# Performance work log

Measured on AMD Instinct MI355X. Metric: run time of the kernel, lower is better.

The kernel has to match this reference:

```python
import jax, jax.numpy as jnp
import numpy as np

B, S, E, H = 4, 2048, 2048, 16
D = E // H  # head_dim = 128
ROPE_BASE = 10000.0


def rope(x, base=ROPE_BASE, offset=0):
    # x: (..., seq, d) with interleaved even/odd rotation
    d = x.shape[-1]
    s = x.shape[-2]
    inv_freq = base ** (-jnp.arange(0, d, 2, dtype=jnp.float32) / d)  # (d/2,)
    pos = jnp.arange(offset, s + offset, dtype=jnp.float32)  # (s,)
    ang = pos[:, None] * inv_freq  # (s, d/2)
    sin, cos = jnp.sin(ang), jnp.cos(ang)
    xe, xo = x[..., 0::2], x[..., 1::2]
    re = xe * cos - xo * sin
    ro = xe * sin + xo * cos
    return jnp.stack([re, ro], axis=-1).reshape(x.shape)


def setup_inputs() -> dict:
    key = jax.random.key(0)
    ks = jax.random.split(key, 9)
    w = lambda k, shp: jax.random.normal(k, shp, dtype=jnp.float32) * 0.02
    return {
        "x": jax.random.normal(ks[0], (B, S, E), dtype=jnp.float32),
        "Wq": w(ks[1], (E, E)), "bq": w(ks[2], (E,)),
        "Wk": w(ks[3], (E, E)), "bk": w(ks[4], (E,)),
        "Wv": w(ks[5], (E, E)), "bv": w(ks[6], (E,)),
        "Wo": w(ks[7], (E, E)), "bo": w(ks[8], (E,)),
    }


def reference(x, Wq, bq, Wk, bk, Wv, bv, Wo, bo):
    b, s, _ = x.shape
    scale = D ** -0.5
    # torch Linear: y = x @ W.T + b
    def proj(W, bias):
        y = jnp.einsum('bse,fe->bsf', x, W) + bias
        return y.reshape(b, s, H, D).transpose(0, 2, 1, 3)  # (b, h, s, d)
    q = rope(proj(Wq, bq))
    k = rope(proj(Wk, bk))
    v = proj(Wv, bv)
    attn = jnp.einsum('bhqd,bhkd->bhqk', q, k) * scale  # (b, h, s, s)
    causal = jnp.triu(jnp.ones((s, s), dtype=bool), k=1)
    attn = jnp.where(causal, -jnp.inf, attn)
    attn_weights = jax.nn.softmax(attn, axis=-1)
    out = jnp.einsum('bhqk,bhkd->bhqd', attn_weights, v)
    out = out.transpose(0, 2, 1, 3).reshape(b, s, E)
    return jnp.einsum('bse,fe->bsf', out, Wo) + bo
```

## Files before the change

kernel.cpp:

```cpp
#include <hip/hip_runtime.h>
#include <hip/hip_bf16.h>
#include <stdint.h>

#define B_ 4
#define S_ 2048
#define E_ 2048
#define H_ 16
#define D_ 128
#define M_ (B_ * S_)

typedef unsigned short ushort_t;
typedef unsigned int uint_t;
typedef __attribute__((ext_vector_type(4))) float f32x4;
typedef __attribute__((ext_vector_type(8))) short bf16x8;

__device__ __forceinline__ ushort_t f2bf(float f) {
  uint_t u = __float_as_uint(f);
  u += 0x7FFFu + ((u >> 16) & 1u);
  return (ushort_t)(u >> 16);
}
__device__ __forceinline__ float bf2f(ushort_t h) {
  return __uint_as_float(((uint_t)h) << 16);
}
__device__ __forceinline__ uint_t cvt_pk_bf16(float lo, float hi) {
  uint_t r;
  asm("v_cvt_pk_bf16_f32 %0, %1, %2" : "=v"(r) : "v"(lo), "v"(hi));
  return r;
}

#define GLOAD_LDS16(gp, lp)                                   \
  __builtin_amdgcn_global_load_lds(                           \
      (__attribute__((address_space(1))) void*)(gp),          \
      (__attribute__((address_space(3))) void*)(lp), 16, 0, 0)

__global__ void f32_to_bf16(const float* __restrict__ in, ushort_t* __restrict__ out,
                            size_t n4) {
  const size_t stride = (size_t)gridDim.x * blockDim.x;
  for (size_t i = (size_t)blockIdx.x * blockDim.x + threadIdx.x; i < n4; i += stride) {
    float4 f = ((const float4*)in)[i];
    uint_t lo = (uint_t)f2bf(f.x) | ((uint_t)f2bf(f.y) << 16);
    uint_t hi = (uint_t)f2bf(f.z) | ((uint_t)f2bf(f.w) << 16);
    ((uint2*)out)[i] = make_uint2(lo, hi);
  }
}

__global__ void rope_k(ushort_t* __restrict__ T) {
  const size_t total = (size_t)M_ * (E_ / 8);
  const size_t stride = (size_t)gridDim.x * blockDim.x;
  for (size_t c = (size_t)blockIdx.x * blockDim.x + threadIdx.x; c < total; c += stride) {
    const int row = (int)(c >> 8);
    const int ch = (int)(c & 255);
    const int s = row & (S_ - 1);
    const int p0 = ((ch * 8) & (D_ - 1)) >> 1;
    ushort_t* p = T + ((size_t)row << 11) + ch * 8;
    bf16x8 v = *(bf16x8*)p;
#pragma unroll
    for (int j = 0; j < 4; j++) {
      const int ip = p0 + j;
      const float inv = __expf(-0.14391156963595867f * (float)ip);
      const float ang = (float)s * inv;
      float sn, cs;
      sincosf(ang, &sn, &cs);
      const float xe = bf2f((ushort_t)v[2 * j]);
      const float xo = bf2f((ushort_t)v[2 * j + 1]);
      v[2 * j] = (short)f2bf(xe * cs - xo * sn);
      v[2 * j + 1] = (short)f2bf(xe * sn + xo * cs);
    }
    *(bf16x8*)p = v;
  }
}

__global__ __launch_bounds__(256) void transpose_v(const ushort_t* __restrict__ Vp,
                                                   ushort_t* __restrict__ Vt) {
  const int b = blockIdx.z, h = blockIdx.y;
  const int s0 = blockIdx.x * 64;
  const int tid = threadIdx.x;
  __shared__ ushort_t T[64][136];
#pragma unroll
  for (int i = 0; i < 4; i++) {
    const int c = i * 256 + tid;
    const int s = c >> 4, d8 = c & 15;
    *(bf16x8*)(&T[s][d8 * 8]) =
        *(const bf16x8*)(Vp + (size_t)(b * S_ + s0 + s) * E_ + h * D_ + d8 * 8);
  }
  __syncthreads();
#pragma unroll
  for (int i = 0; i < 4; i++) {
    const int c = i * 256 + tid;
    const int d = c >> 3, s8 = c & 7;
    bf16x8 v;
#pragma unroll
    for (int j = 0; j < 8; j++) v[j] = (short)T[s8 * 8 + j][d];
    *(bf16x8*)(Vt + ((size_t)(b * H_ + h) * D_ + d) * S_ + s0 + s8 * 8) = v;
  }
}

template <int OUTF32>
__global__ __launch_bounds__(256, 2) void gemm_bt(const ushort_t* __restrict__ A,
                                                  const ushort_t* __restrict__ Bw,
                                                  const float* __restrict__ bias,
                                                  void* __restrict__ Cv) {
  __shared__ ushort_t As[128 * 64];
  __shared__ ushort_t Bs[128 * 64];
  const int tid = threadIdx.x;
  const int w = tid >> 6, l = tid & 63, g = l >> 4, ln = l & 15;
  const int wm = w >> 1, wn = w & 1;
  const int flat = blockIdx.y * 16 + blockIdx.x;
  const int swz = (flat & 7) * 128 + (flat >> 3);
  const int m0 = (swz >> 4) * 128, n0 = (swz & 15) * 128;

  f32x4 acc[4][4];
#pragma unroll
  for (int i = 0; i < 4; i++)
#pragma unroll
    for (int j = 0; j < 4; j++)
#pragma unroll
      for (int r = 0; r < 4; r++) acc[i][j][r] = 0.f;

  const ushort_t* Ab = A + (size_t)m0 * E_;
  const ushort_t* Bb = Bw + (size_t)n0 * E_;

  for (int k0 = 0; k0 < E_; k0 += 64) {
    __syncthreads();
#pragma unroll
    for (int i = 0; i < 4; i++) {
      const int c = i * 256 + tid;
      const int row = c >> 3;
      const int gs = (c & 7) ^ (row & 7);
      GLOAD_LDS16(Ab + (size_t)row * E_ + k0 + gs * 8, (char*)As + (i * 256 + w * 64) * 16);
      GLOAD_LDS16(Bb + (size_t)row * E_ + k0 + gs * 8, (char*)Bs + (i * 256 + w * 64) * 16);
    }
    __syncthreads();
#pragma unroll
    for (int kk = 0; kk < 2; kk++) {
      bf16x8 af[4], bfr[4];
#pragma unroll
      for (int mi = 0; mi < 4; mi++) {
        const int row = wm * 64 + mi * 16 + ln;
        const int sl = (kk * 4 + g) ^ (row & 7);
        af[mi] = *(const bf16x8*)(As + row * 64 + sl * 8);
      }
#pragma unroll
      for (int ni = 0; ni < 4; ni++) {
        const int row = wn * 64 + ni * 16 + ln;
        const int sl = (kk * 4 + g) ^ (row & 7);
        bfr[ni] = *(const bf16x8*)(Bs + row * 64 + sl * 8);
      }
#pragma unroll
      for (int mi = 0; mi < 4; mi++)
#pragma unroll
        for (int ni = 0; ni < 4; ni++)
          acc[mi][ni] =
              __builtin_amdgcn_mfma_f32_16x16x32_bf16(af[mi], bfr[ni], acc[mi][ni], 0, 0, 0);
    }
  }

  float bv[4];
#pragma unroll
  for (int ni = 0; ni < 4; ni++) bv[ni] = bias[n0 + wn * 64 + ni * 16 + ln];
#pragma unroll
  for (int mi = 0; mi < 4; mi++)
#pragma unroll
    for (int ni = 0; ni < 4; ni++)
#pragma unroll
      for (int r = 0; r < 4; r++) {
        const float v = acc[mi][ni][r] + bv[ni];
        const size_t row = m0 + wm * 64 + mi * 16 + g * 4 + r;
        const size_t col = n0 + wn * 64 + ni * 16 + ln;
        if (OUTF32)
          ((float*)Cv)[row * E_ + col] = v;
        else
          ((ushort_t*)Cv)[row * E_ + col] = f2bf(v);
      }
}

__global__ __launch_bounds__(256, 2) void attn_fwd(const ushort_t* __restrict__ Q,
                                                   const ushort_t* __restrict__ K,
                                                   const ushort_t* __restrict__ Vt,
                                                   ushort_t* __restrict__ O) {
  const int b = blockIdx.z, h = blockIdx.y;
  const int pair = blockIdx.x;
  const int tid = threadIdx.x;
  const int w = tid >> 6, l = tid & 63, g = l >> 4, ln = l & 15;

  __shared__ ushort_t Ks[2][64 * 128];
  __shared__ ushort_t Vs[2][128 * 64];
  __shared__ ushort_t Ps[4][32 * 64];

  const ushort_t* Kb = K + (size_t)(b * S_) * E_ + h * D_;
  const ushort_t* Vb = Vt + (size_t)(b * H_ + h) * D_ * S_;
  const float scale = 0.08838834764831845f;

#define STAGE_KV(buf, kv0_)                                                      \
  do {                                                                           \
    _Pragma("unroll") for (int i = 0; i < 4; i++) {                              \
      const int c = i * 256 + tid;                                               \
      const int row = c >> 4, sl = c & 15;                                       \
      const int gs = sl ^ (row & 7);                                             \
      GLOAD_LDS16(Kb + (size_t)((kv0_) + row) * E_ + gs * 8,                     \
                  (char*)(&Ks[buf][0]) + (i * 256 + w * 64) * 16);               \
    }                                                                            \
    _Pragma("unroll") for (int i = 0; i < 4; i++) {                              \
      const int c = i * 256 + tid;                                               \
      const int row = c >> 3, sl = c & 7;                                        \
      const int gs = sl ^ (row & 7);                                             \
      GLOAD_LDS16(Vb + (size_t)row * S_ + (kv0_) + gs * 8,                       \
                  (char*)(&Vs[buf][0]) + (i * 256 + w * 64) * 16);               \
    }                                                                            \
  } while (0)

  for (int pass = 0; pass < 2; pass++) {
    const int u = (pass == 0) ? pair : (15 - pair);
    const int q0 = u * 128;
    const int wrow0 = q0 + w * 32;

    bf16x8 qf[2][4];
    {
      const ushort_t* qb = Q + (size_t)(b * S_ + wrow0) * E_ + h * D_;
#pragma unroll
      for (int mi = 0; mi < 2; mi++)
#pragma unroll
        for (int kk = 0; kk < 4; kk++) {
          bf16x8 v = *(const bf16x8*)(qb + (size_t)(mi * 16 + ln) * E_ + kk * 32 + g * 8);
#pragma unroll
          for (int j = 0; j < 8; j++) v[j] = (short)f2bf(bf2f((ushort_t)v[j]) * scale);
          qf[mi][kk] = v;
        }
    }

    f32x4 oacc[2][8];
#pragma unroll
    for (int mi = 0; mi < 2; mi++)
#pragma unroll
      for (int nd = 0; nd < 8; nd++)
#pragma unroll
        for (int r = 0; r < 4; r++) oacc[mi][nd][r] = 0.f;
    float mrun[2], srun[2];
#pragma unroll
    for (int mi = 0; mi < 2; mi++) {
      mrun[mi] = -__builtin_inff();
      srun[mi] = 0.f;
    }

    const int ntu = 2 * u + 2;
    STAGE_KV(0, 0);

    for (int t = 0; t < ntu; t++) {
      const int kv0 = t * 64;
      const int cur = t & 1;
      if (t + 1 < ntu) {
        STAGE_KV(cur ^ 1, kv0 + 64);
        asm volatile("s_waitcnt vmcnt(8)" ::: "memory");
      } else {
        asm volatile("s_waitcnt vmcnt(0)" ::: "memory");
      }
      __builtin_amdgcn_s_barrier();
      __builtin_amdgcn_sched_barrier(0);

      if (kv0 <= wrow0 + 31) {
        const ushort_t* Kst = &Ks[cur][0];
        const ushort_t* Vst = &Vs[cur][0];
        f32x4 sa[2][4];
#pragma unroll
        for (int mi = 0; mi < 2; mi++)
#pragma unroll
          for (int ni = 0; ni < 4; ni++)
#pragma unroll
            for (int r = 0; r < 4; r++) sa[mi][ni][r] = 0.f;
#pragma unroll
        for (int kk = 0; kk < 4; kk++) {
          bf16x8 kf[4];
#pragma unroll
          for (int ni = 0; ni < 4; ni++) {
            const int row = ni * 16 + ln;
            const int sl = (kk * 4 + g) ^ (row & 7);
            kf[ni] = *(const bf16x8*)(Kst + row * 128 + sl * 8);
          }
#pragma unroll
          for (int mi = 0; mi < 2; mi++)
#pragma unroll
            for (int ni = 0; ni < 4; ni++)
              sa[mi][ni] =
                  __builtin_amdgcn_mfma_f32_16x16x32_bf16(kf[ni], qf[mi][kk], sa[mi][ni], 0, 0, 0);
        }
        if (kv0 + 63 > wrow0) {
#pragma unroll
          for (int mi = 0; mi < 2; mi++) {
            const int lim = wrow0 + mi * 16 + ln - kv0;
#pragma unroll
            for (int ni = 0; ni < 4; ni++)
#pragma unroll
              for (int r = 0; r < 4; r++)
                if (ni * 16 + g * 4 + r > lim) sa[mi][ni][r] = -__builtin_inff();
          }
        }
#pragma unroll
        for (int mi = 0; mi < 2; mi++) {
          float vmax = -__builtin_inff();
#pragma unroll
          for (int ni = 0; ni < 4; ni++)
#pragma unroll
            for (int r = 0; r < 4; r++) vmax = fmaxf(vmax, sa[mi][ni][r]);
          vmax = fmaxf(vmax, __shfl_xor(vmax, 16));
          vmax = fmaxf(vmax, __shfl_xor(vmax, 32));
          if (!__all(vmax - mrun[mi] <= 8.0f)) {
            const float mnew = fmaxf(mrun[mi], vmax);
            const float fs = __expf(mrun[mi] - mnew);
            mrun[mi] = mnew;
            srun[mi] *= fs;
#pragma unroll
            for (int nd = 0; nd < 8; nd++)
#pragma unroll
              for (int r = 0; r < 4; r++) oacc[mi][nd][r] *= fs;
          }
          const float m = mrun[mi];
          float psum = 0.f;
#pragma unroll
          for (int ni = 0; ni < 4; ni++) {
            float p0 = __expf(sa[mi][ni][0] - m);
            float p1 = __expf(sa[mi][ni][1] - m);
            float p2 = __expf(sa[mi][ni][2] - m);
            float p3 = __expf(sa[mi][ni][3] - m);
            psum += (p0 + p1) + (p2 + p3);
            const int byteW =
                (((mi * 16 + ln) * 64 + ni * 16 + g * 4) * 2) ^ ((ln & 7) << 4);
            *(uint2*)((char*)(&Ps[w][0]) + byteW) =
                make_uint2(cvt_pk_bf16(p0, p1), cvt_pk_bf16(p2, p3));
          }
          psum += __shfl_xor(psum, 16);
          psum += __shfl_xor(psum, 32);
          srun[mi] += psum;
        }
        asm volatile("s_waitcnt lgkmcnt(0)" ::: "memory");
        __builtin_amdgcn_sched_barrier(0);
#pragma unroll
        for (int ks = 0; ks < 2; ks++) {
          bf16x8 pf[2];
#pragma unroll
          for (int mi = 0; mi < 2; mi++) {
            const int byteR =
                (((mi * 16 + ln) * 64 + ks * 32 + g * 8) * 2) ^ ((ln & 7) << 4);
            pf[mi] = *(const bf16x8*)((const char*)(&Ps[w][0]) + byteR);
          }
#pragma unroll
          for (int nd = 0; nd < 8; nd++) {
            const int row = nd * 16 + ln;
            const int sl = (ks * 4 + g) ^ (row & 7);
            const bf16x8 vf = *(const bf16x8*)(Vst + row * 64 + sl * 8);
#pragma unroll
            for (int mi = 0; mi < 2; mi++)
              oacc[mi][nd] =
                  __builtin_amdgcn_mfma_f32_16x16x32_bf16(vf, pf[mi], oacc[mi][nd], 0, 0, 0);
          }
        }
      }
      __builtin_amdgcn_s_barrier();
    }

    {
      ushort_t* Ob = O + (size_t)(b * S_ + wrow0) * E_ + h * D_;
#pragma unroll
      for (int mi = 0; mi < 2; mi++) {
        const float inv = 1.0f / srun[mi];
#pragma unroll
        for (int nd = 0; nd < 8; nd++) {
          const uint_t lo = cvt_pk_bf16(oacc[mi][nd][0] * inv, oacc[mi][nd][1] * inv);
          const uint_t hi = cvt_pk_bf16(oacc[mi][nd][2] * inv, oacc[mi][nd][3] * inv);
          *(uint2*)(Ob + (size_t)(mi * 16 + ln) * E_ + nd * 16 + g * 4) = make_uint2(lo, hi);
        }
      }
    }
  }
#undef STAGE_KV
}

extern "C" void kernel_launch(void* const* d_in, const int* in_sizes, int n_in,
                              void* d_out, int out_size, void* d_ws, size_t ws_size,
                              hipStream_t stream) {
  const float* x = (const float*)d_in[0];
  const float* Wq = (const float*)d_in[1];
  const float* bq = (const float*)d_in[2];
  const float* Wk = (const float*)d_in[3];
  const float* bk = (const float*)d_in[4];
  const float* Wv = (const float*)d_in[5];
  const float* bv = (const float*)d_in[6];
  const float* Wo = (const float*)d_in[7];
  const float* bo = (const float*)d_in[8];
  float* out = (float*)d_out;

  ushort_t* ws = (ushort_t*)d_ws;
  const size_t SZ = (size_t)M_ * E_;
  const size_t WSZ = (size_t)E_ * E_;
  ushort_t* xb = ws;
  ushort_t* Qb = ws + SZ;
  ushort_t* Kb = ws + 2 * SZ;
  ushort_t* Vb = ws + 3 * SZ;
  ushort_t* Vtb = ws + 4 * SZ;
  ushort_t* Wqb = ws + 5 * SZ;
  ushort_t* Wkb = Wqb + WSZ;
  ushort_t* Wvb = Wkb + WSZ;
  ushort_t* Wob = Wvb + WSZ;
  ushort_t* Ob = xb;

  f32_to_bf16<<<2048, 256, 0, stream>>>(x, xb, SZ / 4);
  f32_to_bf16<<<1024, 256, 0, stream>>>(Wq, Wqb, WSZ / 4);
  f32_to_bf16<<<1024, 256, 0, stream>>>(Wk, Wkb, WSZ / 4);
  f32_to_bf16<<<1024, 256, 0, stream>>>(Wv, Wvb, WSZ / 4);
  f32_to_bf16<<<1024, 256, 0, stream>>>(Wo, Wob, WSZ / 4);

  dim3 gg(16, 64);
  gemm_bt<0><<<gg, 256, 0, stream>>>(xb, Wqb, bq, Qb);
  gemm_bt<0><<<gg, 256, 0, stream>>>(xb, Wkb, bk, Kb);
  gemm_bt<0><<<gg, 256, 0, stream>>>(xb, Wvb, bv, Vb);

  rope_k<<<2048, 256, 0, stream>>>(Qb);
  rope_k<<<2048, 256, 0, stream>>>(Kb);
  transpose_v<<<dim3(32, H_, B_), 256, 0, stream>>>(Vb, Vtb);

  attn_fwd<<<dim3(8, H_, B_), 256, 0, stream>>>(Qb, Kb, Vtb, Ob);

  gemm_bt<1><<<gg, 256, 0, stream>>>(Ob, Wob, bo, (void*)out);
}
```

Measured before the change: 470.5 us.

## Use 256x256 GEMM tiles with 4-stage pipeline and fuse RoPE and V transpose into epilogues

Replaces the 128x128 GEMM with a 512-thread 256x256-tile kernel that uses a 4-buffer LDS ring with a two-tile prefetch and raised MFMA priority. RoPE for Q and K and the V transpose are now done in the GEMM epilogue, which removes three separate elementwise kernels and their extra memory traffic. Attention gets s_setprio around its MFMA blocks. The cost is one block per CU with 128KB of LDS, a large register footprint, and strided epilogue stores in the V-transpose mode.

```diff
diff --git a/kernel.cpp b/kernel.cpp
--- a/kernel.cpp
+++ b/kernel.cpp
@@ -44,134 +44,131 @@
   }
 }
 
-__global__ void rope_k(ushort_t* __restrict__ T) {
-  const size_t total = (size_t)M_ * (E_ / 8);
-  const size_t stride = (size_t)gridDim.x * blockDim.x;
-  for (size_t c = (size_t)blockIdx.x * blockDim.x + threadIdx.x; c < total; c += stride) {
-    const int row = (int)(c >> 8);
-    const int ch = (int)(c & 255);
-    const int s = row & (S_ - 1);
-    const int p0 = ((ch * 8) & (D_ - 1)) >> 1;
-    ushort_t* p = T + ((size_t)row << 11) + ch * 8;
-    bf16x8 v = *(bf16x8*)p;
-#pragma unroll
-    for (int j = 0; j < 4; j++) {
-      const int ip = p0 + j;
-      const float inv = __expf(-0.14391156963595867f * (float)ip);
-      const float ang = (float)s * inv;
-      float sn, cs;
-      sincosf(ang, &sn, &cs);
-      const float xe = bf2f((ushort_t)v[2 * j]);
-      const float xo = bf2f((ushort_t)v[2 * j + 1]);
-      v[2 * j] = (short)f2bf(xe * cs - xo * sn);
-      v[2 * j + 1] = (short)f2bf(xe * sn + xo * cs);
-    }
-    *(bf16x8*)p = v;
-  }
-}
-
-__global__ __launch_bounds__(256) void transpose_v(const ushort_t* __restrict__ Vp,
-                                                   ushort_t* __restrict__ Vt) {
-  const int b = blockIdx.z, h = blockIdx.y;
-  const int s0 = blockIdx.x * 64;
-  const int tid = threadIdx.x;
-  __shared__ ushort_t T[64][136];
-#pragma unroll
-  for (int i = 0; i < 4; i++) {
-    const int c = i * 256 + tid;
-    const int s = c >> 4, d8 = c & 15;
-    *(bf16x8*)(&T[s][d8 * 8]) =
-        *(const bf16x8*)(Vp + (size_t)(b * S_ + s0 + s) * E_ + h * D_ + d8 * 8);
-  }
-  __syncthreads();
-#pragma unroll
-  for (int i = 0; i < 4; i++) {
-    const int c = i * 256 + tid;
-    const int d = c >> 3, s8 = c & 7;
-    bf16x8 v;
-#pragma unroll
-    for (int j = 0; j < 8; j++) v[j] = (short)T[s8 * 8 + j][d];
-    *(bf16x8*)(Vt + ((size_t)(b * H_ + h) * D_ + d) * S_ + s0 + s8 * 8) = v;
-  }
-}
-
-template <int OUTF32>
-__global__ __launch_bounds__(256, 2) void gemm_bt(const ushort_t* __restrict__ A,
+template <int MODE>
+__global__ __launch_bounds__(512, 1) void gemm256(const ushort_t* __restrict__ A,
                                                   const ushort_t* __restrict__ Bw,
                                                   const float* __restrict__ bias,
                                                   void* __restrict__ Cv) {
-  __shared__ ushort_t As[128 * 64];
-  __shared__ ushort_t Bs[128 * 64];
+  __shared__ __align__(16) char lds[131072];
   const int tid = threadIdx.x;
   const int w = tid >> 6, l = tid & 63, g = l >> 4, ln = l & 15;
-  const int wm = w >> 1, wn = w & 1;
-  const int flat = blockIdx.y * 16 + blockIdx.x;
-  const int swz = (flat & 7) * 128 + (flat >> 3);
-  const int m0 = (swz >> 4) * 128, n0 = (swz & 15) * 128;
-
-  f32x4 acc[4][4];
-#pragma unroll
-  for (int i = 0; i < 4; i++)
-#pragma unroll
-    for (int j = 0; j < 4; j++)
-#pragma unroll
-      for (int r = 0; r < 4; r++) acc[i][j][r] = 0.f;
+  const int wm = w >> 2, wn = w & 3;
+
+  const int flat = blockIdx.x;
+  const int swz = (flat & 7) * 32 + (flat >> 3);
+  const int m0 = (swz >> 3) * 256, n0 = (swz & 7) * 256;
 
   const ushort_t* Ab = A + (size_t)m0 * E_;
   const ushort_t* Bb = Bw + (size_t)n0 * E_;
 
-  for (int k0 = 0; k0 < E_; k0 += 64) {
-    __syncthreads();
-#pragma unroll
-    for (int i = 0; i < 4; i++) {
-      const int c = i * 256 + tid;
-      const int row = c >> 3;
-      const int gs = (c & 7) ^ (row & 7);
-      GLOAD_LDS16(Ab + (size_t)row * E_ + k0 + gs * 8, (char*)As + (i * 256 + w * 64) * 16);
-      GLOAD_LDS16(Bb + (size_t)row * E_ + k0 + gs * 8, (char*)Bs + (i * 256 + w * 64) * 16);
+  int srcOff[2];
+#pragma unroll
+  for (int i = 0; i < 2; i++) {
+    const int c = i * 512 + tid;
+    const int r2 = c >> 3;
+    const int j = (c & 7) ^ (r2 & 7);
+    const int par = j >> 2, cc = j & 3;
+    srcOff[i] = (2 * r2 + par) * E_ + cc * 8;
+  }
+
+  const int NT = E_ / 32;
+
+  auto STAGE = [&](int t_) {
+    char* dst = lds + (t_ & 3) * 32768;
+#pragma unroll
+    for (int i = 0; i < 2; i++)
+      GLOAD_LDS16(Ab + (size_t)(t_ * 32) + srcOff[i], dst + (i * 512 + w * 64) * 16);
+#pragma unroll
+    for (int i = 0; i < 2; i++)
+      GLOAD_LDS16(Bb + (size_t)(t_ * 32) + srcOff[i], dst + 16384 + (i * 512 + w * 64) * 16);
+  };
+
+  const int r2l = ln >> 1, parl = ln & 1;
+  const int chunk = ((parl << 2) + g) ^ r2l;
+  const int addrA0 = (wm * 64 + r2l) * 128 + chunk * 16;
+  const int addrB0 = 16384 + (wn * 32 + r2l) * 128 + chunk * 16;
+
+  f32x4 acc[8][4];
+#pragma unroll
+  for (int mi = 0; mi < 8; mi++)
+#pragma unroll
+    for (int ni = 0; ni < 4; ni++)
+#pragma unroll
+      for (int r = 0; r < 4; r++) acc[mi][ni][r] = 0.f;
+
+  STAGE(0);
+  STAGE(1);
+
+  for (int t = 0; t < NT; t++) {
+    if (t + 1 < NT)
+      asm volatile("s_waitcnt vmcnt(4)" ::: "memory");
+    else
+      asm volatile("s_waitcnt vmcnt(0)" ::: "memory");
+    __builtin_amdgcn_s_barrier();
+    __builtin_amdgcn_sched_barrier(0);
+    if (t + 2 < NT) STAGE(t + 2);
+
+    const char* bufp = lds + (t & 3) * 32768;
+    bf16x8 af[8], bfr[4];
+#pragma unroll
+    for (int mi = 0; mi < 8; mi++) af[mi] = *(const bf16x8*)(bufp + addrA0 + mi * 1024);
+#pragma unroll
+    for (int ni = 0; ni < 4; ni++) bfr[ni] = *(const bf16x8*)(bufp + addrB0 + ni * 1024);
+
+    __builtin_amdgcn_s_setprio(1);
+#pragma unroll
+    for (int mi = 0; mi < 8; mi++)
+#pragma unroll
+      for (int ni = 0; ni < 4; ni++)
+        acc[mi][ni] = __builtin_amdgcn_mfma_f32_16x16x32_bf16(af[mi], bfr[ni], acc[mi][ni], 0, 0, 0);
+    __builtin_amdgcn_s_setprio(0);
+  }
+
+  float bv[4];
+#pragma unroll
+  for (int ni = 0; ni < 4; ni++) bv[ni] = bias[n0 + wn * 64 + ni * 16 + ln];
+
+#pragma unroll
+  for (int mi = 0; mi < 8; mi++)
+#pragma unroll
+    for (int ni = 0; ni < 4; ni++) {
+      const int col = n0 + wn * 64 + ni * 16 + ln;
+      const int row0 = m0 + wm * 128 + mi * 16 + g * 4;
+      float v[4];
+#pragma unroll
+      for (int r = 0; r < 4; r++) v[r] = acc[mi][ni][r] + bv[ni];
+
+      if (MODE == 1) {
+        float* C = (float*)Cv;
+#pragma unroll
+        for (int r = 0; r < 4; r++) C[(size_t)(row0 + r) * E_ + col] = v[r];
+      } else if (MODE == 2) {
+        const int ip = (col & 127) >> 1;
+        const float invf = exp2f(-0.20762050593046f * ip);
+        const float sgn = (col & 1) ? 1.f : -1.f;
+        ushort_t* C = (ushort_t*)Cv;
+#pragma unroll
+        for (int r = 0; r < 4; r++) {
+          const int s = (row0 + r) & (S_ - 1);
+          float sn, cs;
+          sincosf((float)s * invf, &sn, &cs);
+          const float p = __shfl_xor(v[r], 1);
+          const float res = v[r] * cs + sgn * p * sn;
+          C[(size_t)(row0 + r) * E_ + col] = f2bf(res);
+        }
+      } else if (MODE == 3) {
+        ushort_t* C = (ushort_t*)Cv;
+        const int h = col >> 7, d = col & 127;
+        const int b = row0 >> 11, s0 = row0 & (S_ - 1);
+        const uint_t lo = cvt_pk_bf16(v[0], v[1]);
+        const uint_t hi = cvt_pk_bf16(v[2], v[3]);
+        *(uint2*)(C + (((size_t)(b * H_ + h) * D_ + d) * S_ + s0)) = make_uint2(lo, hi);
+      } else {
+        ushort_t* C = (ushort_t*)Cv;
+#pragma unroll
+        for (int r = 0; r < 4; r++) C[(size_t)(row0 + r) * E_ + col] = f2bf(v[r]);
+      }
     }
-    __syncthreads();
-#pragma unroll
-    for (int kk = 0; kk < 2; kk++) {
-      bf16x8 af[4], bfr[4];
-#pragma unroll
-      for (int mi = 0; mi < 4; mi++) {
-        const int row = wm * 64 + mi * 16 + ln;
-        const int sl = (kk * 4 + g) ^ (row & 7);
-        af[mi] = *(const bf16x8*)(As + row * 64 + sl * 8);
-      }
-#pragma unroll
-      for (int ni = 0; ni < 4; ni++) {
-        const int row = wn * 64 + ni * 16 + ln;
-        const int sl = (kk * 4 + g) ^ (row & 7);
-        bfr[ni] = *(const bf16x8*)(Bs + row * 64 + sl * 8);
-      }
-#pragma unroll
-      for (int mi = 0; mi < 4; mi++)
-#pragma unroll
-        for (int ni = 0; ni < 4; ni++)
-          acc[mi][ni] =
-              __builtin_amdgcn_mfma_f32_16x16x32_bf16(af[mi], bfr[ni], acc[mi][ni], 0, 0, 0);
-    }
-  }
-
-  float bv[4];
-#pragma unroll
-  for (int ni = 0; ni < 4; ni++) bv[ni] = bias[n0 + wn * 64 + ni * 16 + ln];
-#pragma unroll
-  for (int mi = 0; mi < 4; mi++)
-#pragma unroll
-    for (int ni = 0; ni < 4; ni++)
-#pragma unroll
-      for (int r = 0; r < 4; r++) {
-        const float v = acc[mi][ni][r] + bv[ni];
-        const size_t row = m0 + wm * 64 + mi * 16 + g * 4 + r;
-        const size_t col = n0 + wn * 64 + ni * 16 + ln;
-        if (OUTF32)
-          ((float*)Cv)[row * E_ + col] = v;
-        else
-          ((ushort_t*)Cv)[row * E_ + col] = f2bf(v);
-      }
 }
 
 __global__ __launch_bounds__(256, 2) void attn_fwd(const ushort_t* __restrict__ Q,
@@ -267,6 +264,7 @@
           for (int ni = 0; ni < 4; ni++)
 #pragma unroll
             for (int r = 0; r < 4; r++) sa[mi][ni][r] = 0.f;
+        __builtin_amdgcn_s_setprio(1);
 #pragma unroll
         for (int kk = 0; kk < 4; kk++) {
           bf16x8 kf[4];
@@ -283,6 +281,7 @@
               sa[mi][ni] =
                   __builtin_amdgcn_mfma_f32_16x16x32_bf16(kf[ni], qf[mi][kk], sa[mi][ni], 0, 0, 0);
         }
+        __builtin_amdgcn_s_setprio(0);
         if (kv0 + 63 > wrow0) {
 #pragma unroll
           for (int mi = 0; mi < 2; mi++) {
@@ -333,6 +332,7 @@
         }
         asm volatile("s_waitcnt lgkmcnt(0)" ::: "memory");
         __builtin_amdgcn_sched_barrier(0);
+        __builtin_amdgcn_s_setprio(1);
 #pragma unroll
         for (int ks = 0; ks < 2; ks++) {
           bf16x8 pf[2];
@@ -353,12 +353,13 @@
                   __builtin_amdgcn_mfma_f32_16x16x32_bf16(vf, pf[mi], oacc[mi][nd], 0, 0, 0);
           }
         }
+        __builtin_amdgcn_s_setprio(0);
       }
       __builtin_amdgcn_s_barrier();
     }
 
     {
-      ushort_t* Ob = O + (size_t)(b * S_ + wrow0) * E_ + h * D_;
+      ushort_t* Ob = O + (size_t)(b * S_ + q0 + w * 32) * E_ + h * D_;
 #pragma unroll
       for (int mi = 0; mi < 2; mi++) {
         const float inv = 1.0f / srun[mi];
@@ -394,7 +395,6 @@
   ushort_t* xb = ws;
   ushort_t* Qb = ws + SZ;
   ushort_t* Kb = ws + 2 * SZ;
-  ushort_t* Vb = ws + 3 * SZ;
   ushort_t* Vtb = ws + 4 * SZ;
   ushort_t* Wqb = ws + 5 * SZ;
   ushort_t* Wkb = Wqb + WSZ;
@@ -408,16 +408,11 @@
   f32_to_bf16<<<1024, 256, 0, stream>>>(Wv, Wvb, WSZ / 4);
   f32_to_bf16<<<1024, 256, 0, stream>>>(Wo, Wob, WSZ / 4);
 
-  dim3 gg(16, 64);
-  gemm_bt<0><<<gg, 256, 0, stream>>>(xb, Wqb, bq, Qb);
-  gemm_bt<0><<<gg, 256, 0, stream>>>(xb, Wkb, bk, Kb);
-  gemm_bt<0><<<gg, 256, 0, stream>>>(xb, Wvb, bv, Vb);
-
-  rope_k<<<2048, 256, 0, stream>>>(Qb);
-  rope_k<<<2048, 256, 0, stream>>>(Kb);
-  transpose_v<<<dim3(32, H_, B_), 256, 0, stream>>>(Vb, Vtb);
+  gemm256<2><<<256, 512, 0, stream>>>(xb, Wqb, bq, Qb);
+  gemm256<2><<<256, 512, 0, stream>>>(xb, Wkb, bk, Kb);
+  gemm256<3><<<256, 512, 0, stream>>>(xb, Wvb, bv, Vtb);
 
   attn_fwd<<<dim3(8, H_, B_), 256, 0, stream>>>(Qb, Kb, Vtb, Ob);
 
-  gemm_bt<1><<<gg, 256, 0, stream>>>(Ob, Wob, bo, (void*)out);
-}
+  gemm256<1><<<256, 512, 0, stream>>>(Ob, Wob, bo, (void*)out);
+}
```

Result: slower. 490.4 us (+4.2%).
